# Kernel tuning notes

Measured on AMD Instinct MI355X. Metric: run time of the kernel, lower is better.

Reference implementation:

```python
import jax, jax.numpy as jnp
import numpy as np

NUM_HEADS = 16
NUM_KV_HEADS = 4
HEAD_DIM = 80
EMBED_DIM = 1280
EPS = 1e-6
NEG_INF = -1e30


def rms_norm(x, w):
    # per-head RMSNorm over last dim, computed in fp32 like the torch module
    xf = x.astype(jnp.float32)
    var = jnp.mean(xf * xf, axis=-1, keepdims=True)
    return (w * (xf * jax.lax.rsqrt(var + EPS))).astype(x.dtype)


def rotate_half(x):
    x1, x2 = jnp.split(x, 2, axis=-1)
    return jnp.concatenate([-x2, x1], axis=-1)


def apply_rope(x, freqs):
    # x: [T, H, hd], freqs: [T, hd]
    cos = jnp.cos(freqs)[:, None, :].astype(jnp.float32)
    sin = jnp.sin(freqs)[:, None, :].astype(jnp.float32)
    xf = x.astype(jnp.float32)
    return (xf * cos + rotate_half(xf) * sin).astype(x.dtype)


def setup_inputs() -> dict:
    key = jax.random.key(0)
    ks = jax.random.split(key, 6)
    T = 4096
    n_seqs = 8  # 8 packed vision sequences of 512 tokens each
    hidden_states = jax.random.normal(ks[0], (T, EMBED_DIM), dtype=jnp.float32)
    cu_seqlens = jnp.arange(n_seqs + 1, dtype=jnp.int32) * (T // n_seqs)
    rotary_pos_emb = jax.random.normal(ks[1], (T, HEAD_DIM), dtype=jnp.float32)
    qkv_rows = (NUM_HEADS + 2 * NUM_KV_HEADS) * HEAD_DIM  # 1920
    w_qkv = jax.random.normal(ks[2], (qkv_rows, EMBED_DIM), dtype=jnp.float32) * (EMBED_DIM ** -0.5)
    w_o = jax.random.normal(ks[3], (EMBED_DIM, NUM_HEADS * HEAD_DIM), dtype=jnp.float32) * ((NUM_HEADS * HEAD_DIM) ** -0.5)
    q_norm_w = jnp.ones((HEAD_DIM,), dtype=jnp.float32)
    k_norm_w = jnp.ones((HEAD_DIM,), dtype=jnp.float32)
    return {
        'hidden_states': hidden_states,
        'cu_seqlens': cu_seqlens,
        'rotary_pos_emb': rotary_pos_emb,
        'w_qkv': w_qkv,
        'w_o': w_o,
        'q_norm_w': q_norm_w,
        'k_norm_w': k_norm_w,
    }


def reference(hidden_states, cu_seqlens, rotary_pos_emb, w_qkv, w_o, q_norm_w, k_norm_w):
    T = hidden_states.shape[0]
    H, KV, hd = NUM_HEADS, NUM_KV_HEADS, HEAD_DIM

    qkv = hidden_states @ w_qkv.T  # [T, (H+2KV)*hd]
    q, k, v = jnp.split(qkv, [H * hd, (H + KV) * hd], axis=-1)
    q = q.reshape(T, H, hd)
    k = k.reshape(T, KV, hd)
    v = v.reshape(T, KV, hd)

    q = rms_norm(q, q_norm_w)
    k = rms_norm(k, k_norm_w)
    q = apply_rope(q, rotary_pos_emb)
    k = apply_rope(k, rotary_pos_emb)

    # GQA: repeat_interleave kv heads to match query heads
    rep = H // KV
    k = jnp.repeat(k, rep, axis=1)  # [T, H, hd]
    v = jnp.repeat(v, rep, axis=1)

    # block-diagonal varlen mask from cu_seqlens
    seg = jnp.searchsorted(cu_seqlens[1:], jnp.arange(T, dtype=cu_seqlens.dtype), side='right')
    mask = seg[:, None] == seg[None, :]  # [T, T]

    scale = hd ** -0.5
    scores = jnp.einsum('thd,shd->hts', q, k) * scale  # [H, T, T]
    scores = jnp.where(mask[None, :, :], scores, NEG_INF)
    probs = jax.nn.softmax(scores, axis=-1)
    attn = jnp.einsum('hts,shd->thd', probs, v)  # [T, H, hd]

    out = attn.reshape(T, H * hd) @ w_o.T  # [T, EMBED_DIM]
    return out
```

## Files before the change

kernel.cpp:

```cpp
#include <hip/hip_runtime.h>
#include <hip/hip_bf16.h>

#define H_Q 16
#define H_KV 4
#define HD 80
#define QKV_ROW 1920
#define K_OFF 1280
#define EMB 1280
#define QT 128
#define KC 64
#define KROW 80
#define PSTR 68
#define VTS 4096

typedef unsigned short u16;
typedef unsigned int u32;
typedef __attribute__((ext_vector_type(8))) short bf16x8;
typedef __attribute__((ext_vector_type(4))) float f32x4;

__device__ inline u16 f2bf(float f) {
  unsigned u = __float_as_uint(f);
  unsigned r = (u + 0x7FFFu + ((u >> 16) & 1u)) >> 16;
  return (u16)r;
}
__device__ inline float bf2f(u16 v) { return __uint_as_float(((unsigned)v) << 16); }

__device__ inline void cvt4(const float* __restrict__ in, u16* __restrict__ out, int q) {
  float4 v = *reinterpret_cast<const float4*>(in + q * 4);
  ushort4 o;
  o.x = f2bf(v.x); o.y = f2bf(v.y); o.z = f2bf(v.z); o.w = f2bf(v.w);
  *reinterpret_cast<ushort4*>(out + q * 4) = o;
}

__global__ __launch_bounds__(256) void prep_kernel(const float* __restrict__ hidden,
                                                   const float* __restrict__ w_qkv,
                                                   const float* __restrict__ w_o,
                                                   const int* __restrict__ cu, int n_seq, int T,
                                                   u16* __restrict__ hid_bf,
                                                   u16* __restrict__ wqkv_bf,
                                                   u16* __restrict__ wo_bf,
                                                   int* __restrict__ seg,
                                                   int nq_hid, int nq_wqkv, int nq_wo) {
  const int i = blockIdx.x * 256 + threadIdx.x;
  if (i < T) {
    int s = 0;
    for (int k = 1; k <= n_seq; ++k) s += (i >= cu[k]) ? 1 : 0;
    seg[i] = s;
  }
  int q = i;
  if (q < nq_hid) { cvt4(hidden, hid_bf, q); return; }
  q -= nq_hid;
  if (q < nq_wqkv) { cvt4(w_qkv, wqkv_bf, q); return; }
  q -= nq_wqkv;
  if (q < nq_wo) cvt4(w_o, wo_bf, q);
}

template <typename OUT, bool VSPLIT>
__global__ __launch_bounds__(256) void gemm_bf16(const u16* __restrict__ A,
                                                 const u16* __restrict__ B,
                                                 OUT* __restrict__ C,
                                                 u16* __restrict__ vt,
                                                 int M, int N, int K, int ldc,
                                                 int gx, int nwg) {
  __shared__ u16 As[3][128 * 32];
  __shared__ u16 Bs[3][128 * 32];
  const int tid = threadIdx.x;
  const int id = blockIdx.x;
  const int sw = (id & 7) * (nwg >> 3) + (id >> 3);
  const int bm = (sw / gx) * 128;
  const int bn = (sw % gx) * 128;
  const int w = tid >> 6;
  const int l = tid & 63;
  const int wr = (w >> 1) * 64, wc = (w & 1) * 64;
  const int fr = l & 15;
  const int fq = l >> 4;
  const int arow = tid >> 2, acol = (tid & 3) * 8;

  f32x4 acc[4][4];
  #pragma unroll
  for (int mi = 0; mi < 4; ++mi)
    #pragma unroll
    for (int ni = 0; ni < 4; ++ni) acc[mi][ni] = (f32x4){0.f, 0.f, 0.f, 0.f};

  #define GSTAGE(buf, k0)                                                             \
    do {                                                                              \
      _Pragma("unroll")                                                               \
      for (int it = 0; it < 2; ++it) {                                                \
        const u16* ga = A + (size_t)(bm + it * 64 + arow) * K + (k0) + acol;          \
        __builtin_amdgcn_global_load_lds(                                             \
            (const __attribute__((address_space(1))) unsigned int*)ga,                \
            (__attribute__((address_space(3))) unsigned int*)&As[buf][it * 2048 + tid * 8], 16, 0, 0); \
        const u16* gb = B + (size_t)(bn + it * 64 + arow) * K + (k0) + acol;          \
        __builtin_amdgcn_global_load_lds(                                             \
            (const __attribute__((address_space(1))) unsigned int*)gb,                \
            (__attribute__((address_space(3))) unsigned int*)&Bs[buf][it * 2048 + tid * 8], 16, 0, 0); \
      }                                                                               \
    } while (0)

  const int nt = K >> 5;
  GSTAGE(0, 0);
  GSTAGE(1, 32);

  int cur = 0;
  for (int t = 0; t < nt; ++t) {
    if (t + 2 < nt) {
      const int nb = (cur + 2) % 3;
      GSTAGE(nb, (t + 2) * 32);
      asm volatile("s_waitcnt vmcnt(8)" ::: "memory");
    } else if (t + 1 < nt) {
      asm volatile("s_waitcnt vmcnt(4)" ::: "memory");
    } else {
      asm volatile("s_waitcnt vmcnt(0)" ::: "memory");
    }
    __builtin_amdgcn_s_barrier();
    __builtin_amdgcn_sched_barrier(0);

    bf16x8 af[4], bfr[4];
    #pragma unroll
    for (int mi = 0; mi < 4; ++mi)
      af[mi] = *reinterpret_cast<const bf16x8*>(&As[cur][(wr + mi * 16 + fr) * 32 + fq * 8]);
    #pragma unroll
    for (int ni = 0; ni < 4; ++ni)
      bfr[ni] = *reinterpret_cast<const bf16x8*>(&Bs[cur][(wc + ni * 16 + fr) * 32 + fq * 8]);
    __builtin_amdgcn_s_setprio(1);
    #pragma unroll
    for (int mi = 0; mi < 4; ++mi)
      #pragma unroll
      for (int ni = 0; ni < 4; ++ni)
        acc[mi][ni] = __builtin_amdgcn_mfma_f32_16x16x32_bf16(af[mi], bfr[ni], acc[mi][ni], 0, 0, 0);
    __builtin_amdgcn_s_setprio(0);

    __builtin_amdgcn_sched_barrier(0);
    __builtin_amdgcn_s_barrier();
    cur = (cur + 1) % 3;
  }
  #undef GSTAGE

  #pragma unroll
  for (int mi = 0; mi < 4; ++mi)
    #pragma unroll
    for (int ni = 0; ni < 4; ++ni) {
      const int col = bn + wc + ni * 16 + fr;
      const int row0 = bm + wr + mi * 16 + fq * 4;
      if (VSPLIT && col >= 1600) {
        ushort4 o;
        o.x = f2bf(acc[mi][ni][0]); o.y = f2bf(acc[mi][ni][1]);
        o.z = f2bf(acc[mi][ni][2]); o.w = f2bf(acc[mi][ni][3]);
        *reinterpret_cast<ushort4*>(&vt[(size_t)(col - 1600) * VTS + row0]) = o;
      } else {
        #pragma unroll
        for (int j = 0; j < 4; ++j) {
          if constexpr (sizeof(OUT) == 2)
            C[(size_t)(row0 + j) * ldc + col] = f2bf(acc[mi][ni][j]);
          else
            C[(size_t)(row0 + j) * ldc + col] = acc[mi][ni][j];
        }
      }
    }
}

__global__ __launch_bounds__(320) void norm_rope_bf(u16* __restrict__ qkv,
                                                    const float* __restrict__ freqs,
                                                    const float* __restrict__ qw,
                                                    const float* __restrict__ kw) {
  const int t = blockIdx.x;
  const int tid = threadIdx.x;
  __shared__ float cs[HD], sn[HD];
  __shared__ float wq[HD], wk[HD];
  __shared__ float xs[5][HD];
  if (tid < HD) {
    const float f = freqs[(size_t)t * HD + tid];
    cs[tid] = __cosf(f);
    sn[tid] = __sinf(f);
    wq[tid] = qw[tid];
    wk[tid] = kw[tid];
  }
  __syncthreads();
  const int w = tid >> 6, lane = tid & 63;
  #pragma unroll
  for (int i = 0; i < 4; ++i) {
    const int hh = w * 4 + i;
    const bool is_q = (hh < H_Q);
    u16* x = qkv + (size_t)t * QKV_ROW + (is_q ? hh * HD : K_OFF + (hh - H_Q) * HD);
    const float* wt = is_q ? wq : wk;
    float a = bf2f(x[lane]);
    float b = (lane < HD - 64) ? bf2f(x[64 + lane]) : 0.0f;
    float ss = a * a + b * b;
    #pragma unroll
    for (int off = 32; off; off >>= 1) ss += __shfl_down(ss, off);
    ss = __shfl(ss, 0);
    const float inv = rsqrtf(ss * (1.0f / HD) + 1e-6f);
    xs[w][lane] = a * inv * wt[lane];
    if (lane < HD - 64) xs[w][64 + lane] = b * inv * wt[64 + lane];
    __syncthreads();
    {
      const int d = lane;
      const float rot = (d < HD / 2) ? -xs[w][d + HD / 2] : xs[w][d - HD / 2];
      x[d] = f2bf(xs[w][d] * cs[d] + rot * sn[d]);
    }
    if (lane < HD - 64) {
      const int d = 64 + lane;
      const float rot = (d < HD / 2) ? -xs[w][d + HD / 2] : xs[w][d - HD / 2];
      x[d] = f2bf(xs[w][d] * cs[d] + rot * sn[d]);
    }
    __syncthreads();
  }
}

__global__ __launch_bounds__(512) void attn_v6(const u16* __restrict__ qkv,
                                               const u16* __restrict__ vt,
                                               const int* __restrict__ seg,
                                               const int* __restrict__ cu,
                                               int T,
                                               u16* __restrict__ attn_bf) {
  __shared__ u16 K_lds[2][KC * KROW + 16];
  __shared__ u16 V_lds[2][96 * 64];
  __shared__ u16 P_lds[QT * PSTR];
  __shared__ int ksegs[2][KC];

  const int t0 = blockIdx.x * QT;
  const int h = blockIdx.y;
  const int kvh = h >> 2;
  const int tid = threadIdx.x;
  const int w = tid >> 6, l = tid & 63;
  const int g = l >> 4, fr = l & 15;

  for (int i = tid; i < 2 * 16 * 32; i += 512) {
    const int b = i >> 9, r = (i >> 5) & 15, c = i & 31;
    ((u32*)V_lds[b])[(80 + r) * 32 + c] = (r == 0) ? 0x3f803f80u : 0u;
  }
  if (tid < 16) { K_lds[0][KC * KROW + tid] = 0; K_lds[1][KC * KROW + tid] = 0; }

  const int s0_ = seg[t0], s1_ = seg[t0 + QT - 1];
  const int kbeg = cu[s0_], kend = cu[s1_ + 1];
  const bool fast = (s0_ == s1_) && (((kend - kbeg) & (KC - 1)) == 0) && ((kbeg & 7) == 0);

  const int qrow = t0 + w * 16 + fr;
  const u16* qp = qkv + (size_t)qrow * QKV_ROW + h * HD;
  bf16x8 qa0 = *reinterpret_cast<const bf16x8*>(qp + g * 8);
  bf16x8 qa1 = *reinterpret_cast<const bf16x8*>(qp + 32 + g * 8);
  bf16x8 qa2 = (g < 2) ? *reinterpret_cast<const bf16x8*>(qp + 64 + g * 8)
                       : (bf16x8)(short)0;
  const int qr0 = t0 + w * 16 + g * 4;
  int qsg[4];
  #pragma unroll
  for (int j = 0; j < 4; ++j) qsg[j] = seg[qr0 + j];

  f32x4 acc[6];
  #pragma unroll
  for (int dt = 0; dt < 6; ++dt) acc[dt] = (f32x4){0.f, 0.f, 0.f, 0.f};
  const float C2 = 0.16130010464f;

  #define ASTAGE(nb, cc)                                                               \
    do {                                                                               \
      for (int i = tid; i < 640; i += 512) {                                           \
        const int kr = i / 10, kc_ = i - kr * 10;                                      \
        const u16* gk = qkv + (size_t)((cc) + kr) * QKV_ROW + K_OFF + kvh * HD + kc_ * 8; \
        __builtin_amdgcn_global_load_lds(                                              \
            (const __attribute__((address_space(1))) u32*)gk,                          \
            (__attribute__((address_space(3))) u32*)&K_lds[nb][i * 8], 16, 0, 0);      \
        const int vr = i >> 3, vs = i & 7;                                             \
        const u16* gv = vt + (size_t)(kvh * HD + vr) * VTS + (cc) + ((vs ^ (vr & 7)) * 8); \
        __builtin_amdgcn_global_load_lds(                                              \
            (const __attribute__((address_space(1))) u32*)gv,                          \
            (__attribute__((address_space(3))) u32*)&V_lds[nb][i * 8], 16, 0, 0);      \
      }                                                                                \
    } while (0)

  #define SSTAGE(nb, cc)                                                               \
    do {                                                                               \
      for (int i = tid; i < KC * 40; i += 512) {                                       \
        const int r = i / 40, ccc = i - r * 40;                                        \
        u32 v = 0;                                                                     \
        if ((cc) + r < kend)                                                           \
          v = reinterpret_cast<const u32*>(qkv + (size_t)((cc) + r) * QKV_ROW + K_OFF + kvh * HD)[ccc]; \
        ((u32*)K_lds[nb])[i] = v;                                                      \
      }                                                                                \
      for (int i = tid; i < HD * KC; i += 512) {                                       \
        const int vr = i >> 6, k = i & 63;                                             \
        u16 v = 0;                                                                     \
        if ((cc) + k < kend)                                                           \
          v = vt[(size_t)(kvh * HD + vr) * VTS + (cc) + k];                            \
        V_lds[nb][vr * 64 + (((k >> 3) ^ (vr & 7)) * 8) + (k & 7)] = v;                \
      }                                                                                \
      if (tid < KC) ksegs[nb][tid] = ((cc) + tid < kend) ? seg[(cc) + tid] : -1;       \
    } while (0)

  if (fast) ASTAGE(0, kbeg); else SSTAGE(0, kbeg);
  __syncthreads();

  int nb = 0;
  for (int c = kbeg; c < kend; c += KC) {
    const int cur = nb;
    nb ^= 1;
    if (c + KC < kend) {
      if (fast) ASTAGE(nb, c + KC); else SSTAGE(nb, c + KC);
    }

    const u16* kb = K_lds[cur];
    f32x4 sacc[4];
    #pragma unroll
    for (int f = 0; f < 4; ++f) {
      const u16* kp = kb + (f * 16 + fr) * KROW;
      bf16x8 b0 = *reinterpret_cast<const bf16x8*>(kp + g * 8);
      bf16x8 b1 = *reinterpret_cast<const bf16x8*>(kp + 32 + g * 8);
      bf16x8 b2 = *reinterpret_cast<const bf16x8*>(kp + 64 + g * 8);
      f32x4 s = (f32x4){0.f, 0.f, 0.f, 0.f};
      s = __builtin_amdgcn_mfma_f32_16x16x32_bf16(qa0, b0, s, 0, 0, 0);
      s = __builtin_amdgcn_mfma_f32_16x16x32_bf16(qa1, b1, s, 0, 0, 0);
      s = __builtin_amdgcn_mfma_f32_16x16x32_bf16(qa2, b2, s, 0, 0, 0);
      sacc[f] = s;
    }

    int ks[4];
    #pragma unroll
    for (int f = 0; f < 4; ++f) ks[f] = qsg[0];
    if (!fast) {
      #pragma unroll
      for (int f = 0; f < 4; ++f) ks[f] = ksegs[cur][f * 16 + fr];
    }
    #pragma unroll
    for (int j = 0; j < 4; ++j) {
      const int prow = w * 16 + g * 4 + j;
      #pragma unroll
      for (int f = 0; f < 4; ++f) {
        float e = sacc[f][j] * C2;
        if (qsg[j] != ks[f]) e = -1e30f;
        const float p = __builtin_exp2f(fminf(e, 43.0f));
        P_lds[prow * PSTR + f * 16 + fr] = f2bf(p);
      }
    }

    const u16* pp = &P_lds[(w * 16 + fr) * PSTR];
    bf16x8 pa0 = *reinterpret_cast<const bf16x8*>(pp + g * 8);
    bf16x8 pa1 = *reinterpret_cast<const bf16x8*>(pp + 32 + g * 8);
    const u16* vb = V_lds[cur];
    #pragma unroll
    for (int dt = 0; dt < 6; ++dt) {
      const int row = dt * 16 + fr;
      const u16* vp = vb + row * 64;
      bf16x8 vb0 = *reinterpret_cast<const bf16x8*>(vp + ((g ^ (fr & 7)) * 8));
      bf16x8 vb1 = *reinterpret_cast<const bf16x8*>(vp + ((((4 + g)) ^ (fr & 7)) * 8));
      acc[dt] = __builtin_amdgcn_mfma_f32_16x16x32_bf16(pa0, vb0, acc[dt], 0, 0, 0);
      acc[dt] = __builtin_amdgcn_mfma_f32_16x16x32_bf16(pa1, vb1, acc[dt], 0, 0, 0);
    }

    __syncthreads();
  }
  #undef ASTAGE
  #undef SSTAGE

  #pragma unroll
  for (int j = 0; j < 4; ++j) {
    const float lsum = __shfl(acc[5][j], l & 48);
    const float il = (lsum > 0.f) ? 1.0f / lsum : 0.f;
    const int row = t0 + w * 16 + g * 4 + j;
    #pragma unroll
    for (int dt = 0; dt < 5; ++dt)
      attn_bf[(size_t)row * EMB + h * HD + dt * 16 + fr] = f2bf(acc[dt][j] * il);
  }
}

extern "C" void kernel_launch(void* const* d_in, const int* in_sizes, int n_in,
                              void* d_out, int out_size, void* d_ws, size_t ws_size,
                              hipStream_t stream) {
  const float* hidden = (const float*)d_in[0];
  const int*   cu     = (const int*)d_in[1];
  const float* rope   = (const float*)d_in[2];
  const float* w_qkv  = (const float*)d_in[3];
  const float* w_o    = (const float*)d_in[4];
  const float* qw     = (const float*)d_in[5];
  const float* kw     = (const float*)d_in[6];
  float* out = (float*)d_out;

  const int T = in_sizes[0] / EMB;
  const int n_seq = in_sizes[1] - 1;

  u16* qkv_bf  = (u16*)d_ws;
  u16* hid_bf  = qkv_bf + (size_t)T * QKV_ROW;
  u16* attn_bf = hid_bf;
  u16* wqkv_bf = hid_bf + (size_t)T * EMB;
  u16* wo_bf   = wqkv_bf + (size_t)QKV_ROW * EMB;
  u16* v_t     = wo_bf + (size_t)EMB * EMB;
  int* segb    = (int*)(v_t + (size_t)320 * 4096 + 64);

  const int nq_hid = T * EMB / 4, nq_wqkv = QKV_ROW * EMB / 4, nq_wo = EMB * EMB / 4;
  const int nq_tot = nq_hid + nq_wqkv + nq_wo;
  prep_kernel<<<(nq_tot + 255) / 256, 256, 0, stream>>>(
      hidden, w_qkv, w_o, cu, n_seq, T, hid_bf, wqkv_bf, wo_bf, segb,
      nq_hid, nq_wqkv, nq_wo);

  {
    const int gx = 15, nwg = gx * (T / 128);
    gemm_bf16<u16, true><<<nwg, 256, 0, stream>>>(hid_bf, wqkv_bf, qkv_bf, v_t,
                                                  T, QKV_ROW, EMB, QKV_ROW, gx, nwg);
  }
  norm_rope_bf<<<T, 320, 0, stream>>>(qkv_bf, rope, qw, kw);
  attn_v6<<<dim3(T / QT, H_Q), 512, 0, stream>>>(qkv_bf, v_t, segb, cu, T, attn_bf);
  {
    const int gx = 10, nwg = gx * (T / 128);
    gemm_bf16<float, false><<<nwg, 256, 0, stream>>>(attn_bf, wo_bf, out, nullptr,
                                                     T, EMB, EMB, EMB, gx, nwg);
  }
}
```

Baseline: 129.1 us.

## Transpose score MFMA and write packed swizzled P tiles per wave

Swaps the MFMA operands so each lane holds four consecutive key scores for one query row. It then converts them to bf16 pairs with v_cvt_pk_bf16_f32 and writes 8-byte chunks into a per-wave XOR-swizzled P buffer, replacing scalar 16-bit LDS stores. The fast path drops the segment masking and the exp clamp. This is meant to cut LDS store count, bank conflicts and VALU work in the softmax-to-PV handoff. It relies on a wave-local s_waitcnt instead of a block barrier, and without the clamp the unnormalised exp could overflow for large scores.

```diff
diff --git a/kernel.cpp b/kernel.cpp
--- a/kernel.cpp
+++ b/kernel.cpp
@@ -10,7 +10,6 @@
 #define QT 128
 #define KC 64
 #define KROW 80
-#define PSTR 68
 #define VTS 4096
 
 typedef unsigned short u16;
@@ -207,7 +206,7 @@
   }
 }
 
-__global__ __launch_bounds__(512) void attn_v6(const u16* __restrict__ qkv,
+__global__ __launch_bounds__(512) void attn_v7(const u16* __restrict__ qkv,
                                                const u16* __restrict__ vt,
                                                const int* __restrict__ seg,
                                                const int* __restrict__ cu,
@@ -215,7 +214,7 @@
                                                u16* __restrict__ attn_bf) {
   __shared__ u16 K_lds[2][KC * KROW + 16];
   __shared__ u16 V_lds[2][96 * 64];
-  __shared__ u16 P_lds[QT * PSTR];
+  __shared__ u32 Pw[8][16 * 36];
   __shared__ int ksegs[2][KC];
 
   const int t0 = blockIdx.x * QT;
@@ -241,10 +240,7 @@
   bf16x8 qa1 = *reinterpret_cast<const bf16x8*>(qp + 32 + g * 8);
   bf16x8 qa2 = (g < 2) ? *reinterpret_cast<const bf16x8*>(qp + 64 + g * 8)
                        : (bf16x8)(short)0;
-  const int qr0 = t0 + w * 16 + g * 4;
-  int qsg[4];
-  #pragma unroll
-  for (int j = 0; j < 4; ++j) qsg[j] = seg[qr0 + j];
+  const int qsgl = seg[qrow];
 
   f32x4 acc[6];
   #pragma unroll
@@ -289,6 +285,10 @@
   if (fast) ASTAGE(0, kbeg); else SSTAGE(0, kbeg);
   __syncthreads();
 
+  const int c3 = (fr & 3) << 2;
+  u32* pw = &Pw[w][0];
+  const int sA = 4 * (g >> 1) + 2 * (g & 1);
+
   int nb = 0;
   for (int c = kbeg; c < kend; c += KC) {
     const int cur = nb;
@@ -306,34 +306,48 @@
       bf16x8 b1 = *reinterpret_cast<const bf16x8*>(kp + 32 + g * 8);
       bf16x8 b2 = *reinterpret_cast<const bf16x8*>(kp + 64 + g * 8);
       f32x4 s = (f32x4){0.f, 0.f, 0.f, 0.f};
-      s = __builtin_amdgcn_mfma_f32_16x16x32_bf16(qa0, b0, s, 0, 0, 0);
-      s = __builtin_amdgcn_mfma_f32_16x16x32_bf16(qa1, b1, s, 0, 0, 0);
-      s = __builtin_amdgcn_mfma_f32_16x16x32_bf16(qa2, b2, s, 0, 0, 0);
+      s = __builtin_amdgcn_mfma_f32_16x16x32_bf16(b0, qa0, s, 0, 0, 0);
+      s = __builtin_amdgcn_mfma_f32_16x16x32_bf16(b1, qa1, s, 0, 0, 0);
+      s = __builtin_amdgcn_mfma_f32_16x16x32_bf16(b2, qa2, s, 0, 0, 0);
       sacc[f] = s;
     }
 
-    int ks[4];
-    #pragma unroll
-    for (int f = 0; f < 4; ++f) ks[f] = qsg[0];
-    if (!fast) {
-      #pragma unroll
-      for (int f = 0; f < 4; ++f) ks[f] = ksegs[cur][f * 16 + fr];
-    }
-    #pragma unroll
-    for (int j = 0; j < 4; ++j) {
-      const int prow = w * 16 + g * 4 + j;
+    if (fast) {
       #pragma unroll
       for (int f = 0; f < 4; ++f) {
-        float e = sacc[f][j] * C2;
-        if (qsg[j] != ks[f]) e = -1e30f;
-        const float p = __builtin_exp2f(fminf(e, 43.0f));
-        P_lds[prow * PSTR + f * 16 + fr] = f2bf(p);
+        const float p0 = __builtin_exp2f(sacc[f][0] * C2);
+        const float p1 = __builtin_exp2f(sacc[f][1] * C2);
+        const float p2 = __builtin_exp2f(sacc[f][2] * C2);
+        const float p3 = __builtin_exp2f(sacc[f][3] * C2);
+        u32 lo, hi;
+        asm("v_cvt_pk_bf16_f32 %0, %1, %2" : "=v"(lo) : "v"(p0), "v"(p1));
+        asm("v_cvt_pk_bf16_f32 %0, %1, %2" : "=v"(hi) : "v"(p2), "v"(p3));
+        const int sel = (4 * f + g) ^ c3;
+        *reinterpret_cast<uint2*>(&pw[fr * 36 + sel * 2]) = make_uint2(lo, hi);
       }
-    }
-
-    const u16* pp = &P_lds[(w * 16 + fr) * PSTR];
-    bf16x8 pa0 = *reinterpret_cast<const bf16x8*>(pp + g * 8);
-    bf16x8 pa1 = *reinterpret_cast<const bf16x8*>(pp + 32 + g * 8);
+    } else {
+      #pragma unroll
+      for (int f = 0; f < 4; ++f) {
+        float pj[4];
+        #pragma unroll
+        for (int j = 0; j < 4; ++j) {
+          const int kk = f * 16 + g * 4 + j;
+          float e = sacc[f][j] * C2;
+          if (qsgl != ksegs[cur][kk]) e = -1e30f;
+          pj[j] = __builtin_exp2f(e);
+        }
+        u32 lo, hi;
+        asm("v_cvt_pk_bf16_f32 %0, %1, %2" : "=v"(lo) : "v"(pj[0]), "v"(pj[1]));
+        asm("v_cvt_pk_bf16_f32 %0, %1, %2" : "=v"(hi) : "v"(pj[2]), "v"(pj[3]));
+        const int sel = (4 * f + g) ^ c3;
+        *reinterpret_cast<uint2*>(&pw[fr * 36 + sel * 2]) = make_uint2(lo, hi);
+      }
+    }
+    asm volatile("s_waitcnt lgkmcnt(0)" ::: "memory");
+    __builtin_amdgcn_sched_barrier(0);
+    bf16x8 pa0 = *reinterpret_cast<const bf16x8*>(&pw[fr * 36 + ((sA ^ c3) * 2)]);
+    bf16x8 pa1 = *reinterpret_cast<const bf16x8*>(&pw[fr * 36 + (((8 + sA) ^ c3) * 2)]);
+
     const u16* vb = V_lds[cur];
     #pragma unroll
     for (int dt = 0; dt < 6; ++dt) {
@@ -396,7 +410,7 @@
                                                   T, QKV_ROW, EMB, QKV_ROW, gx, nwg);
   }
   norm_rope_bf<<<T, 320, 0, stream>>>(qkv_bf, rope, qw, kw);
-  attn_v6<<<dim3(T / QT, H_Q), 512, 0, stream>>>(qkv_bf, v_t, segb, cu, T, attn_bf);
+  attn_v7<<<dim3(T / QT, H_Q), 512, 0, stream>>>(qkv_bf, v_t, segb, cu, T, attn_bf);
   {
     const int gx = 10, nwg = gx * (T / 128);
     gemm_bf16<float, false><<<nwg, 256, 0, stream>>>(attn_bf, wo_bf, out, nullptr,
```

Result: faster. 121.5 us (-5.9%).
